# Performance work log

Hardware: AMD Instinct MI355X
Metric: run time of the kernel (lower is better)

## Reference

```python
import jax, jax.numpy as jnp
import numpy as np

B, S, H = 2, 2048, 2048
NH, D_CKV, D_CQ, DR, DHV = 16, 512, 768, 64, 128
DH = H // NH            # 128 per-head content dim
SCALE = (DR + DH) ** -0.5


def apply_rope(x, freq):
    # x: [b, nh, s, d], freq: [s, d//2] angles; rotate interleaved pairs
    cos = jnp.cos(freq)
    sin = jnp.sin(freq)
    x1 = x[..., 0::2]
    x2 = x[..., 1::2]
    o1 = x1 * cos - x2 * sin
    o2 = x1 * sin + x2 * cos
    return jnp.stack([o1, o2], axis=-1).reshape(x.shape)


def setup_inputs() -> dict:
    key = jax.random.key(0)
    ks = jax.random.split(key, 16)
    w = lambda k, shape: jax.random.normal(k, shape, jnp.float32) * 0.02
    x = jax.random.normal(ks[0], (B, S, H), jnp.float32)
    # rotary angles: pos * inv_freq, shape [S, DR//2]
    inv = 1.0 / (10000.0 ** (jnp.arange(0, DR, 2, dtype=jnp.float32) / DR))
    freq = jnp.arange(S, dtype=jnp.float32)[:, None] * inv[None, :]
    mask = jnp.tril(jnp.ones((S, S), dtype=bool))[None, None]  # causal
    return {
        'x': x, 'freq': freq, 'mask': mask,
        'w_dq': w(ks[1], (H, D_CQ)),          'b_dq': jnp.zeros((D_CQ,), jnp.float32),
        'w_uq': w(ks[2], (D_CQ, NH * DH)),    'b_uq': jnp.zeros((NH * DH,), jnp.float32),
        'w_qr': w(ks[3], (D_CQ, NH * DR)),    'b_qr': jnp.zeros((NH * DR,), jnp.float32),
        'w_dkv': w(ks[4], (H, D_CKV)),        'b_dkv': jnp.zeros((D_CKV,), jnp.float32),
        'w_ukv': w(ks[5], (D_CKV, NH * (DH + DHV))), 'b_ukv': jnp.zeros((NH * (DH + DHV),), jnp.float32),
        'w_kr': w(ks[6], (H, DR)),            'b_kr': jnp.zeros((DR,), jnp.float32),
        'w_o': w(ks[7], (NH * DHV, H)),       'b_o': jnp.zeros((H,), jnp.float32),
    }


def reference(x, freq, mask, w_dq, b_dq, w_uq, b_uq, w_qr, b_qr,
              w_dkv, b_dkv, w_ukv, b_ukv, w_kr, b_kr, w_o, b_o):
    b, s, _ = x.shape
    # query branch: low-rank compression then up-projection
    c_q = x @ w_dq + b_dq                                   # [b,s,d_cq]
    q_c = (c_q @ w_uq + b_uq).reshape(b, s, NH, DH).transpose(0, 2, 1, 3)
    q_r = (c_q @ w_qr + b_qr).reshape(b, s, NH, DR).transpose(0, 2, 1, 3)
    q_r = apply_rope(q_r, freq)
    q = jnp.concatenate([q_c, q_r], axis=-1)               # [b,nh,s,dh+dr]
    # key/value branch: shared kv latent + shared rope key
    c_kv = x @ w_dkv + b_dkv                                # [b,s,d_ckv]
    kv_c = (c_kv @ w_ukv + b_ukv).reshape(b, s, NH, DH + DHV)
    k_c = kv_c[..., :DH].transpose(0, 2, 1, 3)              # [b,nh,s,dh]
    v_c = kv_c[..., DH:].transpose(0, 2, 1, 3)              # [b,nh,s,dhv]
    k_r = (x @ w_kr + b_kr).reshape(b, s, 1, DR).transpose(0, 2, 1, 3)
    k_r = apply_rope(k_r, freq)
    k_r = jnp.broadcast_to(k_r, (b, NH, s, DR))
    k = jnp.concatenate([k_c, k_r], axis=-1)               # [b,nh,s,dh+dr]
    # manual attention
    scores = jnp.einsum('bhsd,bhtd->bhst', q, k) * SCALE
    scores = jnp.where(mask, scores, -jnp.inf)
    attn = jax.nn.softmax(scores, axis=-1)
    out = jnp.einsum('bhst,bhtv->bhsv', attn, v_c)
    out = out.transpose(0, 2, 1, 3).reshape(b, s, NH * DHV)
    return out @ w_o + b_o
```

## Files before the change

kernel.cpp:

```cpp
#include <hip/hip_runtime.h>
#include <cstdint>
#include <cstddef>

#define S_LEN 2048
#define SCALE_F 0.07216878364870323f

typedef __attribute__((ext_vector_type(8))) short short8;
typedef __attribute__((ext_vector_type(4))) float f32x4;
typedef __attribute__((ext_vector_type(16))) float f32x16;
typedef __attribute__((ext_vector_type(4))) unsigned short ushort4v;

__device__ __forceinline__ unsigned short f2bf(float f) {
  unsigned int u = __builtin_bit_cast(unsigned int, f);
  u += 0x7FFFu + ((u >> 16) & 1u);
  return (unsigned short)(u >> 16);
}
__device__ __forceinline__ float bf2f(unsigned short h) {
  unsigned int u = ((unsigned int)h) << 16;
  return __builtin_bit_cast(float, u);
}
__device__ __forceinline__ unsigned int cvt_pk_bf16(float lo, float hi) {
  unsigned int r;
  asm("v_cvt_pk_bf16_f32 %0, %1, %2" : "=v"(r) : "v"(lo), "v"(hi));
  return r;
}

typedef const __attribute__((address_space(1))) void* gas_ptr;
typedef __attribute__((address_space(3))) void* las_ptr;
__device__ __forceinline__ void gload16(const void* g, void* l) {
  __builtin_amdgcn_global_load_lds((gas_ptr)g, (las_ptr)l, 16, 0, 0);
}


__device__ __forceinline__ void transpose_tile(
    const float* __restrict__ src, unsigned short* __restrict__ dst,
    int K, int N, int kb, int nb) {
  __shared__ __align__(16) unsigned short tile[64][72];
  const int tid = threadIdx.x;
  #pragma unroll
  for (int i = 0; i < 4; ++i) {
    int idx = i * 256 + tid;
    int row = idx >> 4, c4 = (idx & 15) << 2;
    const float4 v = *reinterpret_cast<const float4*>(&src[(size_t)(kb + row) * N + nb + c4]);
    tile[row][c4 + 0] = f2bf(v.x);
    tile[row][c4 + 1] = f2bf(v.y);
    tile[row][c4 + 2] = f2bf(v.z);
    tile[row][c4 + 3] = f2bf(v.w);
  }
  __syncthreads();
  #pragma unroll
  for (int i = 0; i < 4; ++i) {
    int idx = i * 256 + tid;
    int n = idx >> 4, kc = (idx & 15) << 2;
    ushort4v o = { tile[kc + 0][n], tile[kc + 1][n], tile[kc + 2][n], tile[kc + 3][n] };
    *reinterpret_cast<ushort4v*>(&dst[(size_t)(nb + n) * K + kb + kc]) = o;
  }
}

__global__ __launch_bounds__(256) void k_prep(
    const float* __restrict__ x, const float* __restrict__ freq,
    const float* __restrict__ wdq, const float* __restrict__ wdkv,
    const float* __restrict__ wkr, const float* __restrict__ wuq,
    const float* __restrict__ wqr, const float* __restrict__ wukv,
    const float* __restrict__ wo,
    const float* __restrict__ b_uq, const float* __restrict__ b_qr,
    const float* __restrict__ b_dq, const float* __restrict__ b_dkv,
    const float* __restrict__ b_kr,
    unsigned short* __restrict__ x_bf, unsigned short* __restrict__ wd_t,
    unsigned short* __restrict__ wqc_t, unsigned short* __restrict__ wukv_t,
    unsigned short* __restrict__ wo_t, float* __restrict__ tab,
    float* __restrict__ bcat, float* __restrict__ ball) {
  const int bid = blockIdx.x;
  const int tid = threadIdx.x;
  if (bid < 384) {
    transpose_tile(wdq, wd_t, 2048, 768, (bid / 12) << 6, (bid % 12) << 6);
  } else if (bid < 640) {
    int r = bid - 384;
    transpose_tile(wdkv, wd_t + (size_t)768 * 2048, 2048, 512, (r >> 3) << 6, (r & 7) << 6);
  } else if (bid < 672) {
    int r = bid - 640;
    transpose_tile(wkr, wd_t + (size_t)1280 * 2048, 2048, 64, r << 6, 0);
  } else if (bid < 1056) {
    int r = bid - 672;
    transpose_tile(wuq, wqc_t, 768, 2048, (r >> 5) << 6, (r & 31) << 6);
  } else if (bid < 1248) {
    int r = bid - 1056;
    transpose_tile(wqr, wqc_t + (size_t)2048 * 768, 768, 1024, (r >> 4) << 6, (r & 15) << 6);
  } else if (bid < 1760) {
    int r = bid - 1248;
    transpose_tile(wukv, wukv_t, 512, 4096, (r >> 6) << 6, (r & 63) << 6);
  } else if (bid < 2784) {
    int r = bid - 1760;
    transpose_tile(wo, wo_t, 2048, 2048, (r >> 5) << 6, (r & 31) << 6);
  } else if (bid < 10976) {
    int i = (bid - 2784) * 256 + tid;
    const float4 v = reinterpret_cast<const float4*>(x)[i];
    ushort4v o = { f2bf(v.x), f2bf(v.y), f2bf(v.z), f2bf(v.w) };
    reinterpret_cast<ushort4v*>(x_bf)[i] = o;
  } else if (bid < 11232) {
    int i = (bid - 10976) * 256 + tid;
    float f = freq[i];
    tab[2 * i] = cosf(f);
    tab[2 * i + 1] = sinf(f);
  } else {
    int i = (bid - 11232) * 256 + tid;
    if (i < 2048) bcat[i] = b_uq[i];
    else if (i < 3072) bcat[i] = b_qr[i - 2048];
    else if (i < 3840) ball[i - 3072] = b_dq[i - 3072];
    else if (i < 4352) ball[i - 3072] = b_dkv[i - 3840];
    else if (i < 4416) ball[i - 3072] = b_kr[i - 4352];
  }
}

__global__ void k_rope_kr(const unsigned short* __restrict__ src, int src_stride,
                          const float* __restrict__ tab,
                          unsigned short* __restrict__ out, int npairs) {
  int idx = blockIdx.x * 256 + threadIdx.x;
  if (idx >= npairs) return;
  int bs = idx >> 5, p = idx & 31;
  int s = bs & (S_LEN - 1);
  float c = tab[(s * 32 + p) * 2], sn = tab[(s * 32 + p) * 2 + 1];
  float x1 = bf2f(src[(size_t)bs * src_stride + 2 * p]);
  float x2 = bf2f(src[(size_t)bs * src_stride + 2 * p + 1]);
  out[bs * 64 + 2 * p] = f2bf(x1 * c - x2 * sn);
  out[bs * 64 + 2 * p + 1] = f2bf(x1 * sn + x2 * c);
}

template <int OUT_BF16>
__global__ __launch_bounds__(256) void k_gemm_bt(
    const unsigned short* __restrict__ A, const unsigned short* __restrict__ Bt,
    const float* __restrict__ bias, void* __restrict__ Cout, int M, int N, int K,
    int lda, int ldc) {
  __shared__ __align__(16) unsigned short As[2][128 * 32];
  __shared__ __align__(16) unsigned short Bs[2][128 * 32];
  const int tid = threadIdx.x;
  const int lane = tid & 63, wid = tid >> 6;
  const int wr = wid >> 1, wc = wid & 1;
  const int nwg = gridDim.x * gridDim.y;
  const int id = blockIdx.y * gridDim.x + blockIdx.x;
  const int l = (id & 7) * (nwg >> 3) + (id >> 3);
  const int m0 = (l / gridDim.x) << 7, n0 = (l % gridDim.x) << 7;
  const int l15 = lane & 15, g = lane >> 4;

  const int srow = (wid << 5) + (lane >> 2);
  const int scol = (lane & 3) << 3;
  const unsigned short* aptr0 = &A[(size_t)(m0 + srow) * lda + scol];
  const unsigned short* aptr1 = &A[(size_t)(m0 + srow + 16) * lda + scol];
  int br0 = n0 + srow;      if (br0 >= N) br0 = N - 1;
  int br1 = n0 + srow + 16; if (br1 >= N) br1 = N - 1;
  const unsigned short* bptr0 = &Bt[(size_t)br0 * K + scol];
  const unsigned short* bptr1 = &Bt[(size_t)br1 * K + scol];
  const int lofs0 = ((wid << 1) + 0) << 9;
  const int lofs1 = ((wid << 1) + 1) << 9;

  f32x4 acc[4][4];
  #pragma unroll
  for (int m = 0; m < 4; ++m)
    #pragma unroll
    for (int n = 0; n < 4; ++n) acc[m][n] = f32x4{0.f, 0.f, 0.f, 0.f};

  gload16(aptr0, &As[0][lofs0]);
  gload16(aptr1, &As[0][lofs1]);
  gload16(bptr0, &Bs[0][lofs0]);
  gload16(bptr1, &Bs[0][lofs1]);
  __syncthreads();

  int cur = 0;
  for (int k0 = 0; k0 < K; k0 += 32) {
    const int nxt = cur ^ 1;
    if (k0 + 32 < K) {
      gload16(aptr0 + k0 + 32, &As[nxt][lofs0]);
      gload16(aptr1 + k0 + 32, &As[nxt][lofs1]);
      gload16(bptr0 + k0 + 32, &Bs[nxt][lofs0]);
      gload16(bptr1 + k0 + 32, &Bs[nxt][lofs1]);
    }
    short8 af[4], bfr[4];
    #pragma unroll
    for (int m = 0; m < 4; ++m)
      af[m] = *reinterpret_cast<const short8*>(
          &As[cur][(((wr << 6) + (m << 4) + l15) << 5) + (g << 3)]);
    #pragma unroll
    for (int n = 0; n < 4; ++n)
      bfr[n] = *reinterpret_cast<const short8*>(
          &Bs[cur][(((wc << 6) + (n << 4) + l15) << 5) + (g << 3)]);
    __builtin_amdgcn_s_setprio(1);
    #pragma unroll
    for (int m = 0; m < 4; ++m)
      #pragma unroll
      for (int n = 0; n < 4; ++n)
        acc[m][n] = __builtin_amdgcn_mfma_f32_16x16x32_bf16(af[m], bfr[n], acc[m][n], 0, 0, 0);
    __builtin_amdgcn_s_setprio(0);
    __syncthreads();
    cur = nxt;
  }
  #pragma unroll
  for (int n = 0; n < 4; ++n) {
    int col = n0 + (wc << 6) + (n << 4) + l15;
    if (col >= N) continue;
    float bv = bias[col];
    #pragma unroll
    for (int m = 0; m < 4; ++m) {
      int rowb = m0 + (wr << 6) + (m << 4) + (g << 2);
      #pragma unroll
      for (int r = 0; r < 4; ++r) {
        float v = acc[m][n][r] + bv;
        if (OUT_BF16)
          reinterpret_cast<unsigned short*>(Cout)[(size_t)(rowb + r) * ldc + col] = f2bf(v);
        else
          reinterpret_cast<float*>(Cout)[(size_t)(rowb + r) * ldc + col] = v;
      }
    }
  }
}

__global__ __launch_bounds__(512, 2) void k_mla_attn(
    const unsigned short* __restrict__ q_raw, const unsigned short* __restrict__ kv_raw,
    const unsigned short* __restrict__ krro, const float* __restrict__ tab,
    unsigned short* __restrict__ attn_out) {
  __shared__ __align__(16) unsigned char smem[73728];
  unsigned short* KcB = reinterpret_cast<unsigned short*>(smem);
  unsigned short* VtB = reinterpret_cast<unsigned short*>(smem + 32768);
  float* Msh = reinterpret_cast<float*>(smem);

  const int tid = threadIdx.x;
  const int lane = tid & 63, w = tid >> 6;
  const int s = w & 3, e = w >> 2;
  const int l31 = lane & 31, hi = lane >> 5;
  const int hi8 = hi << 3;
  const int bid = blockIdx.x;
  const int bh = bid & 31, b = bh >> 4, h = bh & 15;
  const int uu = (bid >> 5) & 7;
  const int chunk = (bid >> 8) ? (15 - uu) : uu;
  const size_t bsb = (size_t)b * S_LEN;

  const int vkv = l31;
  const int vg = (w << 1) | hi;
  const int krow0 = (s << 3) + (lane >> 4);
  const int kunit = lane & 15;

  const int q0 = (chunk << 7) + (s << 5);
  const int srow = q0 + l31;
  const int ntb = (chunk << 2) + 4;
  const int U = ntb >> 1;
  const int nt_w = (q0 + 63) >> 5;

  short8 qf[12];
  {
    const size_t qrow = (bsb + q0 + l31) * 3072;
    #pragma unroll
    for (int ks = 0; ks < 8; ++ks) {
      short8 rv = *reinterpret_cast<const short8*>(&q_raw[qrow + h * 128 + ks * 16 + hi8]);
      union { unsigned short us[8]; short8 v; } uq;
      #pragma unroll
      for (int j = 0; j < 8; ++j)
        uq.us[j] = f2bf(bf2f((unsigned short)rv[j]) * SCALE_F);
      qf[ks] = uq.v;
    }
    #pragma unroll
    for (int f = 0; f < 4; ++f) {
      short8 rv = *reinterpret_cast<const short8*>(
          &q_raw[qrow + 2048 + h * 64 + f * 16 + hi8]);
      int pi0 = 8 * f + 4 * hi;
      union { unsigned short us[8]; short8 v; } uq;
      #pragma unroll
      for (int j = 0; j < 4; ++j) {
        float c = tab[(srow * 32 + pi0 + j) * 2];
        float sn = tab[(srow * 32 + pi0 + j) * 2 + 1];
        float x1 = bf2f((unsigned short)rv[2 * j]);
        float x2 = bf2f((unsigned short)rv[2 * j + 1]);
        uq.us[2 * j] = f2bf((x1 * c - x2 * sn) * SCALE_F);
        uq.us[2 * j + 1] = f2bf((x1 * sn + x2 * c) * SCALE_F);
      }
      qf[8 + f] = uq.v;
    }
  }

  f32x16 acc[4];
  #pragma unroll
  for (int a = 0; a < 4; ++a)
    #pragma unroll
    for (int r = 0; r < 16; ++r) acc[a][r] = 0.f;
  float mrun = -1e30f, lsum = 0.f;

  {
    const int ts = e;
    gload16(&kv_raw[(bsb + (ts << 5) + krow0) * 4096 + h * 256 + (kunit ^ (krow0 & 15)) * 8],
            &KcB[(ts << 12) + ((s << 3) << 7)]);
    gload16(&kv_raw[(bsb + (ts << 5) + krow0 + 4) * 4096 + h * 256 + (kunit ^ ((krow0 + 4) & 15)) * 8],
            &KcB[(ts << 12) + (((s << 3) + 4) << 7)]);
    int4 v0 = *reinterpret_cast<const int4*>(&kv_raw[(bsb + vkv) * 4096 + h * 256 + 128 + vg * 8]);
    int4 v1 = *reinterpret_cast<const int4*>(&kv_raw[(bsb + 32 + vkv) * 4096 + h * 256 + 128 + vg * 8]);
    const unsigned short* p0 = reinterpret_cast<const unsigned short*>(&v0);
    const unsigned short* p1 = reinterpret_cast<const unsigned short*>(&v1);
    #pragma unroll
    for (int j = 0; j < 8; ++j) VtB[0 * 5120 + (vg * 8 + j) * 40 + vkv] = p0[j];
    #pragma unroll
    for (int j = 0; j < 8; ++j) VtB[1 * 5120 + (vg * 8 + j) * 40 + vkv] = p1[j];
  }
  __syncthreads();

  for (int u = 0; u < U; ++u) {
    {
      int tsK = (u << 1) + 2 + e;
      if (tsK < ntb) {
        int buf = tsK & 3;
        gload16(&kv_raw[(bsb + (tsK << 5) + krow0) * 4096 + h * 256 + (kunit ^ (krow0 & 15)) * 8],
                &KcB[(buf << 12) + ((s << 3) << 7)]);
        gload16(&kv_raw[(bsb + (tsK << 5) + krow0 + 4) * 4096 + h * 256 + (kunit ^ ((krow0 + 4) & 15)) * 8],
                &KcB[(buf << 12) + (((s << 3) + 4) << 7)]);
      }
    }
    int4 vA, vB;
    const int tA = (u << 1) + 2, tB = (u << 1) + 3;
    const bool doA = tA < ntb, doB = tB < ntb;
    if (doA) vA = *reinterpret_cast<const int4*>(
        &kv_raw[(bsb + (tA << 5) + vkv) * 4096 + h * 256 + 128 + vg * 8]);
    if (doB) vB = *reinterpret_cast<const int4*>(
        &kv_raw[(bsb + (tB << 5) + vkv) * 4096 + h * 256 + 128 + vg * 8]);

    const int t = (u << 1) + e;
    if (t < nt_w) {
      const int kvb = t << 5;
      const int kbuf = t & 3;
      short8 krf[4];
      #pragma unroll
      for (int f = 0; f < 4; ++f)
        krf[f] = *reinterpret_cast<const short8*>(
            &krro[(bsb + kvb + l31) * 64 + f * 16 + hi8]);

      f32x16 sca, scb;
      #pragma unroll
      for (int r = 0; r < 16; ++r) { sca[r] = 0.f; scb[r] = 0.f; }
      __builtin_amdgcn_s_setprio(1);
      #pragma unroll
      for (int j = 0; j < 4; ++j) {
        short8 k0 = *reinterpret_cast<const short8*>(
            &KcB[(kbuf << 12) + (l31 << 7) + ((((2 * (2 * j)) | hi) ^ (l31 & 15)) << 3)]);
        sca = __builtin_amdgcn_mfma_f32_32x32x16_bf16(k0, qf[2 * j], sca, 0, 0, 0);
        short8 k1 = *reinterpret_cast<const short8*>(
            &KcB[(kbuf << 12) + (l31 << 7) + ((((2 * (2 * j + 1)) | hi) ^ (l31 & 15)) << 3)]);
        scb = __builtin_amdgcn_mfma_f32_32x32x16_bf16(k1, qf[2 * j + 1], scb, 0, 0, 0);
      }
      sca = __builtin_amdgcn_mfma_f32_32x32x16_bf16(krf[0], qf[8], sca, 0, 0, 0);
      scb = __builtin_amdgcn_mfma_f32_32x32x16_bf16(krf[1], qf[9], scb, 0, 0, 0);
      sca = __builtin_amdgcn_mfma_f32_32x32x16_bf16(krf[2], qf[10], sca, 0, 0, 0);
      scb = __builtin_amdgcn_mfma_f32_32x32x16_bf16(krf[3], qf[11], scb, 0, 0, 0);
      __builtin_amdgcn_s_setprio(0);
      f32x16 sc = sca + scb;

      if (kvb + 31 > q0) {
        #pragma unroll
        for (int r = 0; r < 16; ++r) {
          int kv = kvb + (r & 3) + ((r >> 2) << 3) + (hi << 2);
          if (kv > srow) sc[r] = -1e30f;
        }
      }
      float m0 = fmaxf(fmaxf(sc[0], sc[1]), fmaxf(sc[2], sc[3]));
      float m1 = fmaxf(fmaxf(sc[4], sc[5]), fmaxf(sc[6], sc[7]));
      float m2 = fmaxf(fmaxf(sc[8], sc[9]), fmaxf(sc[10], sc[11]));
      float m3 = fmaxf(fmaxf(sc[12], sc[13]), fmaxf(sc[14], sc[15]));
      float tmax = fmaxf(fmaxf(m0, m1), fmaxf(m2, m3));
      tmax = fmaxf(tmax, __shfl_xor(tmax, 32));

      bool rescale = !__all(tmax <= mrun + 8.f);
      float scold = 1.f;
      if (rescale) {
        float mm = fmaxf(mrun, tmax);
        scold = __expf(mrun - mm);
        mrun = mm;
      }
      float pe[16];
      float ts = 0.f;
      #pragma unroll
      for (int r = 0; r < 16; ++r) { pe[r] = __expf(sc[r] - mrun); ts += pe[r]; }
      ts += __shfl_xor(ts, 32);
      lsum = lsum * scold + ts;

      if (rescale) {
        #pragma unroll
        for (int a = 0; a < 4; ++a)
          #pragma unroll
          for (int r = 0; r < 16; ++r) acc[a][r] *= scold;
      }
      #pragma unroll
      for (int ks = 0; ks < 2; ++ks) {
        unsigned int X0 = cvt_pk_bf16(pe[8 * ks + 0], pe[8 * ks + 1]);
        unsigned int X1 = cvt_pk_bf16(pe[8 * ks + 2], pe[8 * ks + 3]);
        unsigned int Y0 = cvt_pk_bf16(pe[8 * ks + 4], pe[8 * ks + 5]);
        unsigned int Y1 = cvt_pk_bf16(pe[8 * ks + 6], pe[8 * ks + 7]);
        unsigned int send0 = hi ? X0 : Y0;
        unsigned int send1 = hi ? X1 : Y1;
        unsigned int recv0 = (unsigned int)__shfl_xor((int)send0, 32);
        unsigned int recv1 = (unsigned int)__shfl_xor((int)send1, 32);
        union { unsigned int u[4]; short8 v; } pa;
        pa.u[0] = hi ? recv0 : X0;
        pa.u[1] = hi ? recv1 : X1;
        pa.u[2] = hi ? Y0 : recv0;
        pa.u[3] = hi ? Y1 : recv1;
        __builtin_amdgcn_s_setprio(1);
        #pragma unroll
        for (int a = 0; a < 4; ++a) {
          short8 va = *reinterpret_cast<const short8*>(
              &VtB[kbuf * 5120 + (32 * a + l31) * 40 + ks * 16 + hi8]);
          acc[a] = __builtin_amdgcn_mfma_f32_32x32x16_bf16(va, pa.v, acc[a], 0, 0, 0);
        }
        __builtin_amdgcn_s_setprio(0);
      }
    }

    if (doA) {
      const unsigned short* pv = reinterpret_cast<const unsigned short*>(&vA);
      #pragma unroll
      for (int j = 0; j < 8; ++j) VtB[(tA & 3) * 5120 + (vg * 8 + j) * 40 + vkv] = pv[j];
    }
    if (doB) {
      const unsigned short* pv = reinterpret_cast<const unsigned short*>(&vB);
      #pragma unroll
      for (int j = 0; j < 8; ++j) VtB[(tB & 3) * 5120 + (vg * 8 + j) * 40 + vkv] = pv[j];
    }
    __syncthreads();
  }

  if (e == 1) {
    #pragma unroll
    for (int a = 0; a < 4; ++a)
      #pragma unroll
      for (int r = 0; r < 16; ++r) {
        int v = 32 * a + (r & 3) + ((r >> 2) << 3) + (hi << 2);
        Msh[((s << 7) + v) * 33 + l31] = acc[a][r];
      }
    if (hi == 0) {
      Msh[16896 + ((s << 5) + l31) * 2 + 0] = mrun;
      Msh[16896 + ((s << 5) + l31) * 2 + 1] = lsum;
    }
  }
  __syncthreads();
  if (e == 0) {
    float m1 = Msh[16896 + ((s << 5) + l31) * 2 + 0];
    float l1 = Msh[16896 + ((s << 5) + l31) * 2 + 1];
    float mm = fmaxf(mrun, m1);
    float ea = __expf(mrun - mm), eb = __expf(m1 - mm);
    float linv = 1.f / (lsum * ea + l1 * eb);
    float al = ea * linv, be = eb * linv;
    #pragma unroll
    for (int a = 0; a < 4; ++a)
      #pragma unroll
      for (int r = 0; r < 16; ++r) {
        int v = 32 * a + (r & 3) + ((r >> 2) << 3) + (hi << 2);
        float part = Msh[((s << 7) + v) * 33 + l31];
        acc[a][r] = acc[a][r] * al + part * be;
      }
    unsigned int* Tb = reinterpret_cast<unsigned int*>(smem) + s * 4224;
    #pragma unroll
    for (int a = 0; a < 4; ++a)
      #pragma unroll
      for (int j = 0; j < 8; ++j) {
        unsigned int word = cvt_pk_bf16(acc[a][2 * j], acc[a][2 * j + 1]);
        int wc = 16 * a + 2 * hi + (j & 1) + 4 * (j >> 1);
        Tb[l31 * 68 + wc] = word;
      }
    const unsigned char* Tbb = reinterpret_cast<const unsigned char*>(Tb);
    #pragma unroll
    for (int u2 = 0; u2 < 8; ++u2) {
      int qr = (u2 << 2) + (lane >> 4);
      int4 rd = *reinterpret_cast<const int4*>(&Tbb[qr * 272 + (lane & 15) * 16]);
      *reinterpret_cast<int4*>(
          &attn_out[(bsb + q0 + qr) * 2048 + h * 128 + (lane & 15) * 8]) = rd;
    }
  }
}


extern "C" void kernel_launch(void* const* d_in, const int* in_sizes, int n_in,
                              void* d_out, int out_size, void* d_ws, size_t ws_size,
                              hipStream_t stream) {
  (void)in_sizes; (void)n_in; (void)out_size; (void)ws_size;
  const float* x = (const float*)d_in[0];
  const float* freq = (const float*)d_in[1];
  const float* w_dq = (const float*)d_in[3];
  const float* b_dq = (const float*)d_in[4];
  const float* w_uq = (const float*)d_in[5];
  const float* b_uq = (const float*)d_in[6];
  const float* w_qr = (const float*)d_in[7];
  const float* b_qr = (const float*)d_in[8];
  const float* w_dkv = (const float*)d_in[9];
  const float* b_dkv = (const float*)d_in[10];
  const float* w_ukv = (const float*)d_in[11];
  const float* b_ukv = (const float*)d_in[12];
  const float* w_kr = (const float*)d_in[13];
  const float* b_kr = (const float*)d_in[14];
  const float* w_o = (const float*)d_in[15];
  const float* b_o = (const float*)d_in[16];

  char* ws = (char*)d_ws;
  size_t off = 0;
  auto alloc = [&](size_t bytes) {
    char* p = ws + off;
    off += (bytes + 255) & ~(size_t)255;
    return p;
  };
  unsigned short* x_bf   = (unsigned short*)alloc((size_t)4096 * 2048 * 2);
  unsigned short* wd_t   = (unsigned short*)alloc((size_t)1344 * 2048 * 2);
  unsigned short* wqc_t  = (unsigned short*)alloc((size_t)3072 * 768 * 2);
  unsigned short* wukv_t = (unsigned short*)alloc((size_t)4096 * 512 * 2);
  unsigned short* wo_t   = (unsigned short*)alloc((size_t)2048 * 2048 * 2);
  float* tab             = (float*)alloc((size_t)2048 * 32 * 2 * 4);
  float* bcat            = (float*)alloc((size_t)3072 * 4);
  float* ball            = (float*)alloc((size_t)1344 * 4);
  unsigned short* c_all  = (unsigned short*)alloc((size_t)4096 * 1344 * 2);
  unsigned short* krro   = (unsigned short*)alloc((size_t)4096 * 64 * 2);
  unsigned short* q_raw  = (unsigned short*)alloc((size_t)4096 * 3072 * 2);
  unsigned short* kv_raw = (unsigned short*)alloc((size_t)4096 * 4096 * 2);
  unsigned short* attn   = (unsigned short*)alloc((size_t)4096 * 2048 * 2);

  k_prep<<<dim3(11250), dim3(256), 0, stream>>>(
      x, freq, w_dq, w_dkv, w_kr, w_uq, w_qr, w_ukv, w_o,
      b_uq, b_qr, b_dq, b_dkv, b_kr,
      x_bf, wd_t, wqc_t, wukv_t, wo_t, tab, bcat, ball);

  k_gemm_bt<1><<<dim3(11, 32), dim3(256), 0, stream>>>(
      x_bf, wd_t, ball, c_all, 4096, 1344, 2048, 2048, 1344);
  k_rope_kr<<<dim3(512), dim3(256), 0, stream>>>(c_all + 1280, 1344, tab, krro, 4096 * 32);

  k_gemm_bt<1><<<dim3(24, 32), dim3(256), 0, stream>>>(
      c_all, wqc_t, bcat, q_raw, 4096, 3072, 768, 1344, 3072);
  k_gemm_bt<1><<<dim3(32, 32), dim3(256), 0, stream>>>(
      c_all + 768, wukv_t, b_ukv, kv_raw, 4096, 4096, 512, 1344, 4096);

  k_mla_attn<<<dim3(512), dim3(512), 0, stream>>>(q_raw, kv_raw, krro, tab, attn);

  k_gemm_bt<0><<<dim3(16, 32), dim3(256), 0, stream>>>(
      attn, wo_t, b_o, (float*)d_out, 4096, 2048, 2048, 2048, 2048);
}
```

Measured before the change: 288.0 us.

## Emit pre-transposed V from KV GEMM and deepen attention async load pipeline

The KV up-projection GEMM epilogue now writes K content and a transposed V into separate buffers, so the attention kernel no longer transposes V through scalar LDS stores. The attention kernel loads both K and V tiles with async global-to-LDS copies into a six-slot ring, prefetched two tiles ahead. It also double-buffers the rope key fragments in registers and swaps the full barrier for a partial vmcnt wait plus s_barrier. The cost is more LDS per block (96KB), which may limit occupancy, and strided scattered stores in the GEMM epilogue for the V transpose.

```diff
diff --git a/kernel.cpp b/kernel.cpp
--- a/kernel.cpp
+++ b/kernel.cpp
@@ -126,11 +126,11 @@
   out[bs * 64 + 2 * p + 1] = f2bf(x1 * sn + x2 * c);
 }
 
-template <int OUT_BF16>
+template <int MODE>
 __global__ __launch_bounds__(256) void k_gemm_bt(
     const unsigned short* __restrict__ A, const unsigned short* __restrict__ Bt,
-    const float* __restrict__ bias, void* __restrict__ Cout, int M, int N, int K,
-    int lda, int ldc) {
+    const float* __restrict__ bias, void* __restrict__ Cout,
+    unsigned short* __restrict__ Vt, int M, int N, int K, int lda, int ldc) {
   __shared__ __align__(16) unsigned short As[2][128 * 32];
   __shared__ __align__(16) unsigned short Bs[2][128 * 32];
   const int tid = threadIdx.x;
@@ -204,22 +204,30 @@
       #pragma unroll
       for (int r = 0; r < 4; ++r) {
         float v = acc[m][n][r] + bv;
-        if (OUT_BF16)
-          reinterpret_cast<unsigned short*>(Cout)[(size_t)(rowb + r) * ldc + col] = f2bf(v);
-        else
-          reinterpret_cast<float*>(Cout)[(size_t)(rowb + r) * ldc + col] = v;
+        int row = rowb + r;
+        if (MODE == 0) {
+          reinterpret_cast<float*>(Cout)[(size_t)row * ldc + col] = v;
+        } else if (MODE == 1) {
+          reinterpret_cast<unsigned short*>(Cout)[(size_t)row * ldc + col] = f2bf(v);
+        } else {
+          int hh = col >> 8, dd = col & 255;
+          if (dd < 128)
+            reinterpret_cast<unsigned short*>(Cout)[(size_t)row * 2048 + hh * 128 + dd] = f2bf(v);
+          else
+            Vt[(((size_t)(row >> 11) * 16 + hh) * 128 + (dd - 128)) * 2048 + (row & 2047)] = f2bf(v);
+        }
       }
     }
   }
 }
 
 __global__ __launch_bounds__(512, 2) void k_mla_attn(
-    const unsigned short* __restrict__ q_raw, const unsigned short* __restrict__ kv_raw,
-    const unsigned short* __restrict__ krro, const float* __restrict__ tab,
-    unsigned short* __restrict__ attn_out) {
-  __shared__ __align__(16) unsigned char smem[73728];
+    const unsigned short* __restrict__ q_raw, const unsigned short* __restrict__ kc,
+    const unsigned short* __restrict__ v_t, const unsigned short* __restrict__ krro,
+    const float* __restrict__ tab, unsigned short* __restrict__ attn_out) {
+  __shared__ __align__(16) unsigned char smem[98304];
   unsigned short* KcB = reinterpret_cast<unsigned short*>(smem);
-  unsigned short* VtB = reinterpret_cast<unsigned short*>(smem + 32768);
+  unsigned short* VtB = reinterpret_cast<unsigned short*>(smem + 49152);
   float* Msh = reinterpret_cast<float*>(smem);
 
   const int tid = threadIdx.x;
@@ -233,10 +241,11 @@
   const int chunk = (bid >> 8) ? (15 - uu) : uu;
   const size_t bsb = (size_t)b * S_LEN;
 
-  const int vkv = l31;
-  const int vg = (w << 1) | hi;
   const int krow0 = (s << 3) + (lane >> 4);
   const int kunit = lane & 15;
+  const int vd = (w << 4) + ((lane >> 2) & 15);
+  const int vswz = (lane & 3) ^ ((lane >> 2) & 3);
+  const size_t vtb = ((size_t)(b * 16 + h) * 128 + vd) * 2048;
 
   const int q0 = (chunk << 7) + (s << 5);
   const int srow = q0 + l31;
@@ -282,51 +291,56 @@
     for (int r = 0; r < 16; ++r) acc[a][r] = 0.f;
   float mrun = -1e30f, lsum = 0.f;
 
+  short8 krf_cur[4], krf_nxt[4];
   {
-    const int ts = e;
-    gload16(&kv_raw[(bsb + (ts << 5) + krow0) * 4096 + h * 256 + (kunit ^ (krow0 & 15)) * 8],
-            &KcB[(ts << 12) + ((s << 3) << 7)]);
-    gload16(&kv_raw[(bsb + (ts << 5) + krow0 + 4) * 4096 + h * 256 + (kunit ^ ((krow0 + 4) & 15)) * 8],
-            &KcB[(ts << 12) + (((s << 3) + 4) << 7)]);
-    int4 v0 = *reinterpret_cast<const int4*>(&kv_raw[(bsb + vkv) * 4096 + h * 256 + 128 + vg * 8]);
-    int4 v1 = *reinterpret_cast<const int4*>(&kv_raw[(bsb + 32 + vkv) * 4096 + h * 256 + 128 + vg * 8]);
-    const unsigned short* p0 = reinterpret_cast<const unsigned short*>(&v0);
-    const unsigned short* p1 = reinterpret_cast<const unsigned short*>(&v1);
-    #pragma unroll
-    for (int j = 0; j < 8; ++j) VtB[0 * 5120 + (vg * 8 + j) * 40 + vkv] = p0[j];
-    #pragma unroll
-    for (int j = 0; j < 8; ++j) VtB[1 * 5120 + (vg * 8 + j) * 40 + vkv] = p1[j];
+    #pragma unroll
+    for (int f = 0; f < 4; ++f)
+      krf_cur[f] = *reinterpret_cast<const short8*>(
+          &krro[(bsb + e * 32 + l31) * 64 + f * 16 + hi8]);
+    #pragma unroll
+    for (int i = 0; i < 2; ++i) {
+      const int ts = e + 2 * i;
+      gload16(&kc[(bsb + (ts << 5) + krow0) * 2048 + h * 128 + (kunit ^ (krow0 & 15)) * 8],
+              &KcB[(ts % 6) * 4096 + (s << 3) * 128]);
+      gload16(&kc[(bsb + (ts << 5) + krow0 + 4) * 2048 + h * 128 + (kunit ^ ((krow0 + 4) & 15)) * 8],
+              &KcB[(ts % 6) * 4096 + ((s << 3) + 4) * 128]);
+    }
+    #pragma unroll
+    for (int tv = 0; tv < 4; ++tv)
+      gload16(&v_t[vtb + tv * 32 + vswz * 8], &VtB[(tv % 6) * 4096 + w * 512]);
   }
   __syncthreads();
 
   for (int u = 0; u < U; ++u) {
+    const int t = (u << 1) + e;
     {
-      int tsK = (u << 1) + 2 + e;
-      if (tsK < ntb) {
-        int buf = tsK & 3;
-        gload16(&kv_raw[(bsb + (tsK << 5) + krow0) * 4096 + h * 256 + (kunit ^ (krow0 & 15)) * 8],
-                &KcB[(buf << 12) + ((s << 3) << 7)]);
-        gload16(&kv_raw[(bsb + (tsK << 5) + krow0 + 4) * 4096 + h * 256 + (kunit ^ ((krow0 + 4) & 15)) * 8],
-                &KcB[(buf << 12) + (((s << 3) + 4) << 7)]);
-      }
-    }
-    int4 vA, vB;
-    const int tA = (u << 1) + 2, tB = (u << 1) + 3;
-    const bool doA = tA < ntb, doB = tB < ntb;
-    if (doA) vA = *reinterpret_cast<const int4*>(
-        &kv_raw[(bsb + (tA << 5) + vkv) * 4096 + h * 256 + 128 + vg * 8]);
-    if (doB) vB = *reinterpret_cast<const int4*>(
-        &kv_raw[(bsb + (tB << 5) + vkv) * 4096 + h * 256 + 128 + vg * 8]);
-
-    const int t = (u << 1) + e;
+      int t2 = t + 2; if (t2 > 63) t2 = 63;
+      #pragma unroll
+      for (int f = 0; f < 4; ++f)
+        krf_nxt[f] = *reinterpret_cast<const short8*>(
+            &krro[(bsb + (t2 << 5) + l31) * 64 + f * 16 + hi8]);
+    }
+    {
+      int tsK = (u << 1) + 4 + e;
+      int src = tsK > 63 ? 63 : tsK;
+      int kb = tsK % 6;
+      gload16(&kc[(bsb + (src << 5) + krow0) * 2048 + h * 128 + (kunit ^ (krow0 & 15)) * 8],
+              &KcB[kb * 4096 + (s << 3) * 128]);
+      gload16(&kc[(bsb + (src << 5) + krow0 + 4) * 2048 + h * 128 + (kunit ^ ((krow0 + 4) & 15)) * 8],
+              &KcB[kb * 4096 + ((s << 3) + 4) * 128]);
+    }
+    {
+      int tvA = (u << 1) + 4;
+      int sA = tvA > 63 ? 63 : tvA;
+      gload16(&v_t[vtb + (sA << 5) + vswz * 8], &VtB[(tvA % 6) * 4096 + w * 512]);
+      int tvB = tvA + 1;
+      int sB = tvB > 63 ? 63 : tvB;
+      gload16(&v_t[vtb + (sB << 5) + vswz * 8], &VtB[(tvB % 6) * 4096 + w * 512]);
+    }
+
     if (t < nt_w) {
       const int kvb = t << 5;
-      const int kbuf = t & 3;
-      short8 krf[4];
-      #pragma unroll
-      for (int f = 0; f < 4; ++f)
-        krf[f] = *reinterpret_cast<const short8*>(
-            &krro[(bsb + kvb + l31) * 64 + f * 16 + hi8]);
+      const int kbuf = t % 6;
 
       f32x16 sca, scb;
       #pragma unroll
@@ -335,16 +349,16 @@
       #pragma unroll
       for (int j = 0; j < 4; ++j) {
         short8 k0 = *reinterpret_cast<const short8*>(
-            &KcB[(kbuf << 12) + (l31 << 7) + ((((2 * (2 * j)) | hi) ^ (l31 & 15)) << 3)]);
+            &KcB[kbuf * 4096 + (l31 << 7) + ((((2 * (2 * j)) | hi) ^ (l31 & 15)) << 3)]);
         sca = __builtin_amdgcn_mfma_f32_32x32x16_bf16(k0, qf[2 * j], sca, 0, 0, 0);
         short8 k1 = *reinterpret_cast<const short8*>(
-            &KcB[(kbuf << 12) + (l31 << 7) + ((((2 * (2 * j + 1)) | hi) ^ (l31 & 15)) << 3)]);
+            &KcB[kbuf * 4096 + (l31 << 7) + ((((2 * (2 * j + 1)) | hi) ^ (l31 & 15)) << 3)]);
         scb = __builtin_amdgcn_mfma_f32_32x32x16_bf16(k1, qf[2 * j + 1], scb, 0, 0, 0);
       }
-      sca = __builtin_amdgcn_mfma_f32_32x32x16_bf16(krf[0], qf[8], sca, 0, 0, 0);
-      scb = __builtin_amdgcn_mfma_f32_32x32x16_bf16(krf[1], qf[9], scb, 0, 0, 0);
-      sca = __builtin_amdgcn_mfma_f32_32x32x16_bf16(krf[2], qf[10], sca, 0, 0, 0);
-      scb = __builtin_amdgcn_mfma_f32_32x32x16_bf16(krf[3], qf[11], scb, 0, 0, 0);
+      sca = __builtin_amdgcn_mfma_f32_32x32x16_bf16(krf_cur[0], qf[8], sca, 0, 0, 0);
+      scb = __builtin_amdgcn_mfma_f32_32x32x16_bf16(krf_cur[1], qf[9], scb, 0, 0, 0);
+      sca = __builtin_amdgcn_mfma_f32_32x32x16_bf16(krf_cur[2], qf[10], sca, 0, 0, 0);
+      scb = __builtin_amdgcn_mfma_f32_32x32x16_bf16(krf_cur[3], qf[11], scb, 0, 0, 0);
       __builtin_amdgcn_s_setprio(0);
       f32x16 sc = sca + scb;
 
@@ -401,25 +415,21 @@
         #pragma unroll
         for (int a = 0; a < 4; ++a) {
           short8 va = *reinterpret_cast<const short8*>(
-              &VtB[kbuf * 5120 + (32 * a + l31) * 40 + ks * 16 + hi8]);
+              &VtB[kbuf * 4096 + ((a << 5) + l31) * 32 + ((((ks << 1) | hi) ^ (l31 & 3)) << 3)]);
           acc[a] = __builtin_amdgcn_mfma_f32_32x32x16_bf16(va, pa.v, acc[a], 0, 0, 0);
         }
         __builtin_amdgcn_s_setprio(0);
       }
     }
 
-    if (doA) {
-      const unsigned short* pv = reinterpret_cast<const unsigned short*>(&vA);
-      #pragma unroll
-      for (int j = 0; j < 8; ++j) VtB[(tA & 3) * 5120 + (vg * 8 + j) * 40 + vkv] = pv[j];
-    }
-    if (doB) {
-      const unsigned short* pv = reinterpret_cast<const unsigned short*>(&vB);
-      #pragma unroll
-      for (int j = 0; j < 8; ++j) VtB[(tB & 3) * 5120 + (vg * 8 + j) * 40 + vkv] = pv[j];
-    }
-    __syncthreads();
-  }
+    #pragma unroll
+    for (int f = 0; f < 4; ++f) krf_cur[f] = krf_nxt[f];
+
+    asm volatile("s_waitcnt vmcnt(8) lgkmcnt(0)" ::: "memory");
+    __builtin_amdgcn_s_barrier();
+  }
+
+  __syncthreads();
 
   if (e == 1) {
     #pragma unroll
@@ -510,7 +520,8 @@
   unsigned short* c_all  = (unsigned short*)alloc((size_t)4096 * 1344 * 2);
   unsigned short* krro   = (unsigned short*)alloc((size_t)4096 * 64 * 2);
   unsigned short* q_raw  = (unsigned short*)alloc((size_t)4096 * 3072 * 2);
-  unsigned short* kv_raw = (unsigned short*)alloc((size_t)4096 * 4096 * 2);
+  unsigned short* kc     = (unsigned short*)alloc((size_t)4096 * 2048 * 2);
+  unsigned short* v_t    = (unsigned short*)alloc((size_t)4096 * 2048 * 2);
   unsigned short* attn   = (unsigned short*)alloc((size_t)4096 * 2048 * 2);
 
   k_prep<<<dim3(11250), dim3(256), 0, stream>>>(
@@ -519,16 +530,16 @@
       x_bf, wd_t, wqc_t, wukv_t, wo_t, tab, bcat, ball);
 
   k_gemm_bt<1><<<dim3(11, 32), dim3(256), 0, stream>>>(
-      x_bf, wd_t, ball, c_all, 4096, 1344, 2048, 2048, 1344);
+      x_bf, wd_t, ball, c_all, nullptr, 4096, 1344, 2048, 2048, 1344);
   k_rope_kr<<<dim3(512), dim3(256), 0, stream>>>(c_all + 1280, 1344, tab, krro, 4096 * 32);
 
   k_gemm_bt<1><<<dim3(24, 32), dim3(256), 0, stream>>>(
-      c_all, wqc_t, bcat, q_raw, 4096, 3072, 768, 1344, 3072);
-  k_gemm_bt<1><<<dim3(32, 32), dim3(256), 0, stream>>>(
-      c_all + 768, wukv_t, b_ukv, kv_raw, 4096, 4096, 512, 1344, 4096);
-
-  k_mla_attn<<<dim3(512), dim3(512), 0, stream>>>(q_raw, kv_raw, krro, tab, attn);
+      c_all, wqc_t, bcat, q_raw, nullptr, 4096, 3072, 768, 1344, 3072);
+  k_gemm_bt<2><<<dim3(32, 32), dim3(256), 0, stream>>>(
+      c_all + 768, wukv_t, b_ukv, kc, v_t, 4096, 4096, 512, 1344, 2048);
+
+  k_mla_attn<<<dim3(512), dim3(512), 0, stream>>>(q_raw, kc, v_t, krro, tab, attn);
 
   k_gemm_bt<0><<<dim3(16, 32), dim3(256), 0, stream>>>(
-      attn, wo_t, b_o, (float*)d_out, 4096, 2048, 2048, 2048, 2048);
-}
+      attn, wo_t, b_o, (float*)d_out, nullptr, 4096, 2048, 2048, 2048, 2048);
+}
```

New measurement: 289.9 us. No clear change (+0.6%).
